# Kernel optimization log

Measured on AMD Instinct MI355X. Metric: run time of the kernel, lower is better.

Reference implementation:

```python
import jax, jax.numpy as jnp
import numpy as np

B, T, K, V, D, H = 16, 512, 32, 512, 64, 128


def setup_inputs() -> dict:
    key = jax.random.key(0)
    ks = jax.random.split(key, 10)
    s = lambda k, shape: jax.random.normal(k, shape, jnp.float32) * 0.05
    sequences = jax.random.randint(ks[0], (B, T), 0, V)
    lengths = jax.random.randint(ks[1], (B,), 1, T + 1)
    return dict(
        sequences=sequences,
        lengths=lengths,
        emb=s(ks[2], (V, D)),
        W1=s(ks[3], (D, H)), b1=jnp.zeros((H,), jnp.float32),
        W2=s(ks[4], (H, K * K)), b2=jnp.zeros((K * K,), jnp.float32),
        E1=s(ks[5], (D, H)), e1=jnp.zeros((H,), jnp.float32),
        E2=s(ks[6], (H, K * V)), e2=jnp.zeros((K * V,), jnp.float32),
        init_logits=s(ks[7], (K,)),
    )


def reference(sequences, lengths, emb, W1, b1, W2, b2, E1, e1, E2, e2, init_logits):
    Bc, Tc = sequences.shape
    # shift inputs: start token 0 followed by sequences[:, :-1]
    inputs = jnp.concatenate(
        [jnp.zeros((Bc, 1), sequences.dtype), sequences[:, :-1]], axis=1)
    x = emb[inputs]                                  # (B,T,D)
    # transition net -> (B,T,K,K) row-normalized in log space
    h1 = jax.nn.relu(x @ W1 + b1)
    log_trans = jax.nn.log_softmax((h1 @ W2 + b2).reshape(Bc, Tc, K, K), axis=-1)
    # emission net -> (B,T,K,V), gather observed-token scores
    h2 = jax.nn.relu(x @ E1 + e1)
    log_emit = jax.nn.log_softmax((h2 @ E2 + e2).reshape(Bc, Tc, K, V), axis=-1)
    tgt = jnp.broadcast_to(sequences[:, :, None, None], (Bc, Tc, K, 1))
    emit_scores = jnp.take_along_axis(log_emit, tgt, axis=3)[..., 0]  # (B,T,K)
    init_lp = jax.nn.log_softmax(init_logits)
    alpha0 = init_lp[None, :] + emit_scores[:, 0]    # (B,K)

    def step(alpha, xs):
        lt, es, t = xs                               # (B,K,K),(B,K),()
        new = jax.nn.logsumexp(alpha[:, :, None] + lt, axis=1) + es
        alpha = jnp.where((t < lengths)[:, None], new, alpha)
        return alpha, None

    xs = (jnp.swapaxes(log_trans, 0, 1)[1:],
          jnp.swapaxes(emit_scores, 0, 1)[1:],
          jnp.arange(1, Tc))
    alpha, _ = jax.lax.scan(step, alpha0, xs)
    return -jax.nn.logsumexp(alpha, axis=1)         # (B,) negative log-likelihood
```

## Files before the change

kernel.cpp:

```cpp
#include <hip/hip_runtime.h>
#include <hip/hip_bf16.h>

#define BB 16
#define TT 512
#define KK 32
#define VV 512
#define DD 64
#define HH 128
#define KV (KK*VV)
#define KKK (KK*KK)

#define INV_LN2 1.4426950408889634f
#define LN2 0.6931471805599453f

typedef unsigned short u16;
typedef __attribute__((ext_vector_type(8))) short short8;
typedef __attribute__((ext_vector_type(8))) unsigned short ushort8;
typedef __attribute__((ext_vector_type(16))) float f32x16;
typedef __attribute__((ext_vector_type(4))) unsigned int uint4v;

__device__ __forceinline__ float fexp2(float x) { return __builtin_amdgcn_exp2f(x); }
__device__ __forceinline__ float flog2(float x) { return __builtin_amdgcn_logf(x); }

__device__ __forceinline__ u16 f2bf(float f) {
  unsigned u = __builtin_bit_cast(unsigned, f);
  u += 0x7FFFu + ((u >> 16) & 1u);
  return (u16)(u >> 16);
}
__device__ __forceinline__ float bf2f(u16 v) {
  return __builtin_bit_cast(float, ((unsigned)v) << 16);
}

__device__ __forceinline__ float es_dot(const u16* __restrict__ erow,
                                        const u16* __restrict__ hrow) {
  float a0 = 0.f, a1 = 0.f, a2 = 0.f, a3 = 0.f;
#pragma unroll
  for (int r = 0; r < 8; ++r) {
    short8 ev = ((const short8*)erow)[r];
    short8 hv = ((const short8*)hrow)[r];
    a0 += bf2f((u16)ev[0]) * bf2f((u16)hv[0]);
    a1 += bf2f((u16)ev[1]) * bf2f((u16)hv[1]);
    a2 += bf2f((u16)ev[2]) * bf2f((u16)hv[2]);
    a3 += bf2f((u16)ev[3]) * bf2f((u16)hv[3]);
    a0 += bf2f((u16)ev[4]) * bf2f((u16)hv[4]);
    a1 += bf2f((u16)ev[5]) * bf2f((u16)hv[5]);
    a2 += bf2f((u16)ev[6]) * bf2f((u16)hv[6]);
    a3 += bf2f((u16)ev[7]) * bf2f((u16)hv[7]);
  }
  return (a0 + a1) + (a2 + a3);
}

__device__ __forceinline__ void mul_step(short8 fr0, short8 fr1, int h,
                                         float* D) {
  float e0[8], e1[8];
#pragma unroll
  for (int i2 = 0; i2 < 4; ++i2) {
    float x0 = __shfl_xor(D[i2], 32);
    float y0 = __shfl_xor(D[4 + i2], 32);
    e0[i2] = (h == 0) ? D[i2] : y0;
    e0[4 + i2] = (h == 0) ? x0 : D[4 + i2];
    float x1 = __shfl_xor(D[8 + i2], 32);
    float y1 = __shfl_xor(D[12 + i2], 32);
    e1[i2] = (h == 0) ? D[8 + i2] : y1;
    e1[4 + i2] = (h == 0) ? x1 : D[12 + i2];
  }
  short8 B0, B1;
#pragma unroll
  for (int e = 0; e < 8; ++e) {
    B0[e] = (short)f2bf(e0[e]);
    B1[e] = (short)f2bf(e1[e]);
  }
  f32x16 dn = {};
  dn = __builtin_amdgcn_mfma_f32_32x32x16_bf16(fr0, B0, dn, 0, 0, 0);
  dn = __builtin_amdgcn_mfma_f32_32x32x16_bf16(fr1, B1, dn, 0, 0, 0);
#pragma unroll
  for (int r = 0; r < 16; ++r) D[r] = dn[r];
}

__device__ __forceinline__ void ident_D(int j, int h, float* D) {
#pragma unroll
  for (int r = 0; r < 16; ++r) D[r] = 0.f;
  if (((j >> 2) & 1) == h) D[(j & 3) | ((j >> 3) << 2)] = 1.0f;
}

__global__ __launch_bounds__(256) void k_prep1(
    const float* __restrict__ E2, u16* __restrict__ E2bT,
    const float* __restrict__ W2, u16* __restrict__ W2T,
    const float* __restrict__ emb, const float* __restrict__ W1,
    const float* __restrict__ b1, const float* __restrict__ E1,
    const float* __restrict__ e1, u16* __restrict__ h1b,
    u16* __restrict__ h2b) {
  __shared__ float tl[32][65];
  __shared__ float embs[16][64];
  int tid = threadIdx.x;
  int bid = blockIdx.x;

  if (bid < 1088) {
    const float* src;
    u16* dst;
    size_t srcld;
    int c0, h0;
    if (bid < 1024) {
      c0 = (bid & 255) * 64;
      h0 = (bid >> 8) * 32;
      src = E2;
      dst = E2bT;
      srcld = KV;
    } else {
      int b2i = bid - 1024;
      c0 = (b2i & 15) * 64;
      h0 = (b2i >> 4) * 32;
      src = W2;
      dst = W2T;
      srcld = KKK;
    }
    int r = tid >> 6, c = tid & 63;
#pragma unroll
    for (int rr = 0; rr < 8; ++rr)
      tl[r * 8 + rr][c] = src[(size_t)(h0 + r * 8 + rr) * srcld + c0 + c];
    __syncthreads();
    int cw = tid >> 3, hb = tid & 7;
#pragma unroll
    for (int pass = 0; pass < 2; ++pass) {
      int cc = pass * 32 + cw;
      unsigned lo = (unsigned)f2bf(tl[hb * 4 + 0][cc]) |
                    ((unsigned)f2bf(tl[hb * 4 + 1][cc]) << 16);
      unsigned hi = (unsigned)f2bf(tl[hb * 4 + 2][cc]) |
                    ((unsigned)f2bf(tl[hb * 4 + 3][cc]) << 16);
      uint2 v;
      v.x = lo;
      v.y = hi;
      *(uint2*)(dst + (size_t)(c0 + cc) * HH + h0 + hb * 4) = v;
    }
    return;
  }

  int u0 = (bid - 1088) * 16;
#pragma unroll
  for (int it = 0; it < 4; ++it) {
    int idx = it * 256 + tid;
    embs[idx >> 6][idx & 63] = emb[u0 * DD + idx];
  }
  __syncthreads();
  int h = tid & 127, tl2 = tid >> 7;
  float b1v = b1[h], e1v = e1[h];
#pragma unroll
  for (int it = 0; it < 8; ++it) {
    int tok = it * 2 + tl2;
    float a1 = b1v, a2 = e1v;
#pragma unroll 8
    for (int d = 0; d < DD; ++d) {
      float xv = embs[tok][d];
      a1 += xv * W1[d * HH + h];
      a2 += xv * E1[d * HH + h];
    }
    h1b[(u0 + tok) * HH + h] = f2bf(fmaxf(a1, 0.f));
    h2b[(u0 + tok) * HH + h] = f2bf(fmaxf(a2, 0.f));
  }
}

__global__ __launch_bounds__(256) void k_transmfma(
    const u16* __restrict__ h1b, const u16* __restrict__ W2T,
    const float* __restrict__ b2, float* __restrict__ ltrans) {
  int i = blockIdx.x;
  int w = threadIdx.x >> 6, l = threadIdx.x & 63;
  int tt = blockIdx.y * 4 + w;
  int u0 = tt * 32;
  int h = l >> 5, j = l & 31;

  f32x16 acc = {};
#pragma unroll
  for (int kh = 0; kh < 8; ++kh) {
    short8 A = *(const short8*)(h1b + (u0 + j) * HH + kh * 16 + h * 8);
    short8 Bf = *(const short8*)(W2T + (i * 32 + j) * HH + kh * 16 + h * 8);
    acc = __builtin_amdgcn_mfma_f32_32x32x16_bf16(A, Bf, acc, 0, 0, 0);
  }
  float b2v = b2[i * 32 + j] * INV_LN2;
  float lgv[16], se[16];
#pragma unroll
  for (int r = 0; r < 16; ++r) {
    lgv[r] = acc[r] * INV_LN2 + b2v;
    se[r] = fexp2(lgv[r]);
  }
#pragma unroll
  for (int r = 0; r < 16; ++r) {
#pragma unroll
    for (int d = 1; d < 32; d <<= 1) se[r] += __shfl_xor(se[r], d);
  }
#pragma unroll
  for (int r = 0; r < 16; ++r) {
    int row = (r & 3) + 8 * (r >> 2) + 4 * h;
    ltrans[(u0 + row) * KKK + j * KK + i] = lgv[r] - flog2(se[r]);
  }
}

__global__ __launch_bounds__(256) void k_emit_lse(
    const u16* __restrict__ h2b, const u16* __restrict__ E2bT,
    const float* __restrict__ e2, float* __restrict__ lse2_tab) {
  int k = blockIdx.x;
  int u0 = blockIdx.y * 32;
  int tid = threadIdx.x;
  int w = tid >> 6, l = tid & 63;
  int h = l >> 5, j = l & 31;
  __shared__ float ls[4 * 32];

  short8 A[8];
#pragma unroll
  for (int kh = 0; kh < 8; ++kh)
    A[kh] = *(const short8*)(h2b + (u0 + j) * HH + kh * 16 + h * 8);

  float s[16];
#pragma unroll
  for (int r = 0; r < 16; ++r) s[r] = 0.f;

#pragma unroll
  for (int c = 0; c < 4; ++c) {
    int ct = w * 4 + c;
    int col = k * 512 + ct * 32 + j;
    const u16* bp = E2bT + (size_t)col * HH + h * 8;
    f32x16 acc = {};
#pragma unroll
    for (int kh = 0; kh < 8; ++kh) {
      short8 Bf = *(const short8*)(bp + kh * 16);
      acc = __builtin_amdgcn_mfma_f32_32x32x16_bf16(A[kh], Bf, acc, 0, 0, 0);
    }
    float e2v = e2[col] * INV_LN2;
#pragma unroll
    for (int r = 0; r < 16; ++r) s[r] += fexp2(acc[r] * INV_LN2 + e2v);
  }
#pragma unroll
  for (int r = 0; r < 16; ++r) {
#pragma unroll
    for (int d = 1; d < 32; d <<= 1) s[r] += __shfl_xor(s[r], d);
  }
  if (j == 0) {
#pragma unroll
    for (int r = 0; r < 16; ++r) {
      int row = (r & 3) + 8 * (r >> 2) + 4 * h;
      ls[w * 32 + row] = s[r];
    }
  }
  __syncthreads();
  if (tid < 32) {
    float total = ls[tid] + ls[32 + tid] + ls[64 + tid] + ls[96 + tid];
    lse2_tab[(u0 + tid) * KK + k] = flog2(total);
  }
}

__global__ __launch_bounds__(256) void k_matprod(
    const int* __restrict__ seq, const int* __restrict__ lengths,
    const float* __restrict__ ltrans, const u16* __restrict__ h2b,
    const u16* __restrict__ E2bT, const float* __restrict__ e2,
    const float* __restrict__ lse2, u16* __restrict__ C1,
    float* __restrict__ s1) {
  __shared__ float tmp[4][32 * 33];
  int w = threadIdx.x >> 6, l = threadIdx.x & 63;
  int c = blockIdx.x * 4 + w;
  int b = c >> 7, t0 = (c & 127) * 4;
  int j = l & 31, h = l >> 5;
  int len = lengths[b];
  len = (len < 1) ? 1 : ((len > TT) ? TT : len);
  const int* sb = seq + b * TT;
  int tlo = (t0 < 1) ? 1 : t0;
  int thi = (t0 + 4 < len) ? (t0 + 4) : len;

  u16* op = C1 + (size_t)c * 1024 + j * 32 + h * 16;
  if (tlo >= thi) {
    ushort8 w0v, w1v;
#pragma unroll
    for (int e = 0; e < 8; ++e) {
      w0v[e] = ((h * 16 + e) == j) ? (u16)0x3F80 : (u16)0;
      w1v[e] = ((h * 16 + 8 + e) == j) ? (u16)0x3F80 : (u16)0;
    }
    *(ushort8*)op = w0v;
    *(ushort8*)(op + 8) = w1v;
    if (l == 0) s1[c] = 0.f;
    return;
  }

  short8 fr0s[4], fr1s[4];
  float sacc = 0.f;
#pragma unroll
  for (int s = 0; s < 4; ++s) {
    int t = t0 + s;
    if (t >= 1 && t < len) {
      int u = sb[t - 1], y = sb[t];
      float dot = es_dot(E2bT + (size_t)(j * VV + y) * HH + h * 64,
                         h2b + u * HH + h * 64);
      dot += __shfl_xor(dot, 32);
      float esj = (dot + e2[j * VV + y]) * INV_LN2 - lse2[u * KK + j];
      float m = esj;
#pragma unroll
      for (int d = 1; d < 32; d <<= 1) m = fmaxf(m, __shfl_xor(m, d));
      sacc += m;
      const float4* p4 = (const float4*)(ltrans + u * KKK + j * KK + h * 16);
      float4 q0 = p4[0], q1 = p4[1], q2 = p4[2], q3 = p4[3];
      float lgv[16] = {q0.x, q0.y, q0.z, q0.w, q1.x, q1.y, q1.z, q1.w,
                       q2.x, q2.y, q2.z, q2.w, q3.x, q3.y, q3.z, q3.w};
      float off = esj - m;
#pragma unroll
      for (int e = 0; e < 16; ++e) lgv[e] += off;
      unsigned pk[8];
#pragma unroll
      for (int p = 0; p < 8; ++p)
        pk[p] = (unsigned)f2bf(fexp2(lgv[2 * p])) |
                ((unsigned)f2bf(fexp2(lgv[2 * p + 1])) << 16);
      unsigned rcv[4];
#pragma unroll
      for (int p = 0; p < 4; ++p)
        rcv[p] = (unsigned)__shfl_xor((int)(h == 0 ? pk[4 + p] : pk[p]), 32);
      unsigned f0[4], f1[4];
#pragma unroll
      for (int p = 0; p < 4; ++p) {
        f0[p] = h == 0 ? pk[p] : rcv[p];
        f1[p] = h == 0 ? rcv[p] : pk[4 + p];
      }
      fr0s[s] = __builtin_bit_cast(short8, (uint4v){f0[0], f0[1], f0[2], f0[3]});
      fr1s[s] = __builtin_bit_cast(short8, (uint4v){f1[0], f1[1], f1[2], f1[3]});
    } else {
      ushort8 i0, i1;
#pragma unroll
      for (int e = 0; e < 8; ++e) {
        i0[e] = ((h * 8 + e) == j) ? (u16)0x3F80 : (u16)0;
        i1[e] = ((16 + h * 8 + e) == j) ? (u16)0x3F80 : (u16)0;
      }
      fr0s[s] = __builtin_bit_cast(short8, i0);
      fr1s[s] = __builtin_bit_cast(short8, i1);
    }
  }

  float D[16];
  ident_D(j, h, D);
#pragma unroll
  for (int s = 0; s < 4; ++s) mul_step(fr0s[s], fr1s[s], h, D);

  float mx = D[0];
#pragma unroll
  for (int r = 1; r < 16; ++r) mx = fmaxf(mx, D[r]);
#pragma unroll
  for (int d = 1; d < 64; d <<= 1) mx = fmaxf(mx, __shfl_xor(mx, d));
  float inv = 1.0f / mx;
#pragma unroll
  for (int r = 0; r < 16; ++r) {
    int row = (r & 3) + 8 * (r >> 2) + 4 * h;
    tmp[w][row * 33 + j] = D[r] * inv;
  }
  ushort8 w0v, w1v;
#pragma unroll
  for (int e = 0; e < 8; ++e) {
    w0v[e] = f2bf(tmp[w][j * 33 + h * 16 + e]);
    w1v[e] = f2bf(tmp[w][j * 33 + h * 16 + 8 + e]);
  }
  *(ushort8*)op = w0v;
  *(ushort8*)(op + 8) = w1v;
  if (l == 0) s1[c] = flog2(mx) + sacc;
}

__global__ __launch_bounds__(512) void k_final2(
    const u16* __restrict__ C1, const float* __restrict__ s1,
    const int* __restrict__ seq, const u16* __restrict__ h2b,
    const u16* __restrict__ E2bT, const float* __restrict__ e2,
    const float* __restrict__ lse2, const float* __restrict__ init_logits,
    float* __restrict__ out) {
  __shared__ u16 mats[8][1024];
  __shared__ float scs[8];
  int b = blockIdx.x;
  int w = threadIdx.x >> 6, l = threadIdx.x & 63;
  int j = l & 31, h = l >> 5;

  float D[16];
  ident_D(j, h, D);
  const u16* base = C1 + ((size_t)b * 128 + w * 16) * 1024;
#pragma unroll
  for (int s = 0; s < 16; ++s) {
    short8 fr0 = *(const short8*)(base + s * 1024 + j * 32 + h * 8);
    short8 fr1 = *(const short8*)(base + s * 1024 + j * 32 + h * 8 + 16);
    mul_step(fr0, fr1, h, D);
  }
  float mx = D[0];
#pragma unroll
  for (int r = 1; r < 16; ++r) mx = fmaxf(mx, D[r]);
#pragma unroll
  for (int d = 1; d < 64; d <<= 1) mx = fmaxf(mx, __shfl_xor(mx, d));
  float inv = 1.0f / mx;
#pragma unroll
  for (int r = 0; r < 16; ++r) {
    int row = (r & 3) + 8 * (r >> 2) + 4 * h;
    mats[w][row * 32 + j] = f2bf(D[r] * inv);
  }
  float si = (l < 16) ? s1[b * 128 + w * 16 + l] : 0.f;
#pragma unroll
  for (int d = 1; d < 64; d <<= 1) si += __shfl_xor(si, d);
  if (l == 0) scs[w] = flog2(mx) + si;
  __syncthreads();

  if (w == 0) {
    float D2[16];
    ident_D(j, h, D2);
#pragma unroll
    for (int s = 0; s < 8; ++s) {
      short8 fr0 = *(const short8*)(&mats[s][j * 32 + h * 8]);
      short8 fr1 = *(const short8*)(&mats[s][j * 32 + h * 8 + 16]);
      mul_step(fr0, fr1, h, D2);
    }
    int y0 = seq[b * TT];
    float dot = es_dot(E2bT + (size_t)(j * VV + y0) * HH + h * 64,
                       h2b + h * 64);
    dot += __shfl_xor(dot, 32);
    float esj = (dot + e2[j * VV + y0]) * INV_LN2 - lse2[j];
    float il = init_logits[j] * INV_LN2;
    float m0 = il;
#pragma unroll
    for (int d = 1; d < 32; d <<= 1) m0 = fmaxf(m0, __shfl_xor(m0, d));
    float s0 = fexp2(il - m0);
#pragma unroll
    for (int d = 1; d < 32; d <<= 1) s0 += __shfl_xor(s0, d);
    float lse0 = m0 + flog2(s0);
    float z = il - lse0 + esj;
    float am = z;
#pragma unroll
    for (int d = 1; d < 32; d <<= 1) am = fmaxf(am, __shfl_xor(am, d));
    float a0 = fexp2(z - am);
    float colsum = 0.f;
#pragma unroll
    for (int r = 0; r < 16; ++r) colsum += D2[r];
    float p = a0 * colsum;
#pragma unroll
    for (int d = 1; d < 64; d <<= 1) p += __shfl_xor(p, d);
    float sct = (l < 8) ? scs[l] : 0.f;
#pragma unroll
    for (int d = 1; d < 64; d <<= 1) sct += __shfl_xor(sct, d);
    if (l == 0) out[b] = -LN2 * (flog2(p) + am + sct);
  }
}

extern "C" void kernel_launch(void* const* d_in, const int* in_sizes, int n_in,
                              void* d_out, int out_size, void* d_ws,
                              size_t ws_size, hipStream_t stream) {
  const int* seq = (const int*)d_in[0];
  const int* lengths = (const int*)d_in[1];
  const float* emb = (const float*)d_in[2];
  const float* W1 = (const float*)d_in[3];
  const float* b1 = (const float*)d_in[4];
  const float* W2 = (const float*)d_in[5];
  const float* b2 = (const float*)d_in[6];
  const float* E1 = (const float*)d_in[7];
  const float* e1 = (const float*)d_in[8];
  const float* E2 = (const float*)d_in[9];
  const float* e2 = (const float*)d_in[10];
  const float* init_logits = (const float*)d_in[11];
  float* out = (float*)d_out;

  char* wsb = (char*)d_ws;
  float* ltrans = (float*)(wsb + 0);
  u16* h2b = (u16*)(wsb + 2097152);
  u16* h1b = (u16*)(wsb + 2228224);
  u16* E2bT = (u16*)(wsb + 2359296);
  u16* W2T = (u16*)(wsb + 6553600);
  float* lse2 = (float*)(wsb + 6815744);
  u16* C1 = (u16*)(wsb + 6881280);
  float* s1 = (float*)(wsb + 11075584);

  k_prep1<<<1120, 256, 0, stream>>>(E2, E2bT, W2, W2T, emb, W1, b1, E1, e1,
                                    h1b, h2b);
  k_transmfma<<<dim3(32, 4), 256, 0, stream>>>(h1b, W2T, b2, ltrans);
  k_emit_lse<<<dim3(32, 16), 256, 0, stream>>>(h2b, E2bT, e2, lse2);
  k_matprod<<<512, 256, 0, stream>>>(seq, lengths, ltrans, h2b, E2bT, e2,
                                     lse2, C1, s1);
  k_final2<<<16, 512, 0, stream>>>(C1, s1, seq, h2b, E2bT, e2, lse2,
                                   init_logits, out);
}
```

Measured before the change: 90.32 us.

## Merge table kernels and fold final reduction into matprod via last-block atomic

```diff
diff --git a/kernel.cpp b/kernel.cpp
--- a/kernel.cpp
+++ b/kernel.cpp
@@ -89,11 +89,12 @@
     const float* __restrict__ emb, const float* __restrict__ W1,
     const float* __restrict__ b1, const float* __restrict__ E1,
     const float* __restrict__ e1, u16* __restrict__ h1b,
-    u16* __restrict__ h2b) {
+    u16* __restrict__ h2b, int* __restrict__ cnt) {
   __shared__ float tl[32][65];
   __shared__ float embs[16][64];
   int tid = threadIdx.x;
   int bid = blockIdx.x;
+  if (bid == 0 && tid < BB) cnt[tid] = 0;
 
   if (bid < 1088) {
     const float* src;
@@ -159,14 +160,69 @@
   }
 }
 
-__global__ __launch_bounds__(256) void k_transmfma(
+__global__ __launch_bounds__(256) void k_tables(
     const u16* __restrict__ h1b, const u16* __restrict__ W2T,
-    const float* __restrict__ b2, float* __restrict__ ltrans) {
-  int i = blockIdx.x;
-  int w = threadIdx.x >> 6, l = threadIdx.x & 63;
-  int tt = blockIdx.y * 4 + w;
+    const float* __restrict__ b2, float* __restrict__ ltrans,
+    const u16* __restrict__ h2b, const u16* __restrict__ E2bT,
+    const float* __restrict__ e2, float* __restrict__ lse2_tab) {
+  __shared__ float ls[4 * 32];
+  int bid = blockIdx.x;
+  int tid = threadIdx.x;
+  int w = tid >> 6, l = tid & 63;
+  int h = l >> 5, j = l & 31;
+
+  if (bid < 512) {
+    int k = bid & 31;
+    int u0 = (bid >> 5) * 32;
+
+    short8 A[8];
+#pragma unroll
+    for (int kh = 0; kh < 8; ++kh)
+      A[kh] = *(const short8*)(h2b + (u0 + j) * HH + kh * 16 + h * 8);
+
+    float s[16];
+#pragma unroll
+    for (int r = 0; r < 16; ++r) s[r] = 0.f;
+
+#pragma unroll
+    for (int c = 0; c < 4; ++c) {
+      int ct = w * 4 + c;
+      int col = k * 512 + ct * 32 + j;
+      const u16* bp = E2bT + (size_t)col * HH + h * 8;
+      f32x16 acc = {};
+#pragma unroll
+      for (int kh = 0; kh < 8; ++kh) {
+        short8 Bf = *(const short8*)(bp + kh * 16);
+        acc = __builtin_amdgcn_mfma_f32_32x32x16_bf16(A[kh], Bf, acc, 0, 0, 0);
+      }
+      float e2v = e2[col] * INV_LN2;
+#pragma unroll
+      for (int r = 0; r < 16; ++r) s[r] += fexp2(acc[r] * INV_LN2 + e2v);
+    }
+#pragma unroll
+    for (int r = 0; r < 16; ++r) {
+#pragma unroll
+      for (int d = 1; d < 32; d <<= 1) s[r] += __shfl_xor(s[r], d);
+    }
+    if (j == 0) {
+#pragma unroll
+      for (int r = 0; r < 16; ++r) {
+        int row = (r & 3) + 8 * (r >> 2) + 4 * h;
+        ls[w * 32 + row] = s[r];
+      }
+    }
+    __syncthreads();
+    if (tid < 32) {
+      float total = ls[tid] + ls[32 + tid] + ls[64 + tid] + ls[96 + tid];
+      lse2_tab[(u0 + tid) * KK + k] = flog2(total);
+    }
+    return;
+  }
+
+  int t2 = bid - 512;
+  int i = t2 & 31;
+  int tt = (t2 >> 5) * 4 + w;
   int u0 = tt * 32;
-  int h = l >> 5, j = l & 31;
 
   f32x16 acc = {};
 #pragma unroll
@@ -191,59 +247,6 @@
   for (int r = 0; r < 16; ++r) {
     int row = (r & 3) + 8 * (r >> 2) + 4 * h;
     ltrans[(u0 + row) * KKK + j * KK + i] = lgv[r] - flog2(se[r]);
-  }
-}
-
-__global__ __launch_bounds__(256) void k_emit_lse(
-    const u16* __restrict__ h2b, const u16* __restrict__ E2bT,
-    const float* __restrict__ e2, float* __restrict__ lse2_tab) {
-  int k = blockIdx.x;
-  int u0 = blockIdx.y * 32;
-  int tid = threadIdx.x;
-  int w = tid >> 6, l = tid & 63;
-  int h = l >> 5, j = l & 31;
-  __shared__ float ls[4 * 32];
-
-  short8 A[8];
-#pragma unroll
-  for (int kh = 0; kh < 8; ++kh)
-    A[kh] = *(const short8*)(h2b + (u0 + j) * HH + kh * 16 + h * 8);
-
-  float s[16];
-#pragma unroll
-  for (int r = 0; r < 16; ++r) s[r] = 0.f;
-
-#pragma unroll
-  for (int c = 0; c < 4; ++c) {
-    int ct = w * 4 + c;
-    int col = k * 512 + ct * 32 + j;
-    const u16* bp = E2bT + (size_t)col * HH + h * 8;
-    f32x16 acc = {};
-#pragma unroll
-    for (int kh = 0; kh < 8; ++kh) {
-      short8 Bf = *(const short8*)(bp + kh * 16);
-      acc = __builtin_amdgcn_mfma_f32_32x32x16_bf16(A[kh], Bf, acc, 0, 0, 0);
-    }
-    float e2v = e2[col] * INV_LN2;
-#pragma unroll
-    for (int r = 0; r < 16; ++r) s[r] += fexp2(acc[r] * INV_LN2 + e2v);
-  }
-#pragma unroll
-  for (int r = 0; r < 16; ++r) {
-#pragma unroll
-    for (int d = 1; d < 32; d <<= 1) s[r] += __shfl_xor(s[r], d);
-  }
-  if (j == 0) {
-#pragma unroll
-    for (int r = 0; r < 16; ++r) {
-      int row = (r & 3) + 8 * (r >> 2) + 4 * h;
-      ls[w * 32 + row] = s[r];
-    }
-  }
-  __syncthreads();
-  if (tid < 32) {
-    float total = ls[tid] + ls[32 + tid] + ls[64 + tid] + ls[96 + tid];
-    lse2_tab[(u0 + tid) * KK + k] = flog2(total);
   }
 }
 
@@ -252,17 +255,21 @@
     const float* __restrict__ ltrans, const u16* __restrict__ h2b,
     const u16* __restrict__ E2bT, const float* __restrict__ e2,
     const float* __restrict__ lse2, u16* __restrict__ C1,
-    float* __restrict__ s1) {
+    float* __restrict__ s1, int* __restrict__ cnt,
+    const float* __restrict__ init_logits, float* __restrict__ out) {
   __shared__ float tmp[4][32 * 33];
+  __shared__ u16 mats[4][1024];
+  __shared__ float scs[4];
+  __shared__ int lastflag;
   int w = threadIdx.x >> 6, l = threadIdx.x & 63;
   int c = blockIdx.x * 4 + w;
-  int b = c >> 7, t0 = (c & 127) * 4;
+  int b = c >> 6, t0 = (c & 63) * 8;
   int j = l & 31, h = l >> 5;
   int len = lengths[b];
   len = (len < 1) ? 1 : ((len > TT) ? TT : len);
   const int* sb = seq + b * TT;
   int tlo = (t0 < 1) ? 1 : t0;
-  int thi = (t0 + 4 < len) ? (t0 + 4) : len;
+  int thi = (t0 + 8 < len) ? (t0 + 8) : len;
 
   u16* op = C1 + (size_t)c * 1024 + j * 32 + h * 16;
   if (tlo >= thi) {
@@ -275,102 +282,100 @@
     *(ushort8*)op = w0v;
     *(ushort8*)(op + 8) = w1v;
     if (l == 0) s1[c] = 0.f;
-    return;
-  }
-
-  short8 fr0s[4], fr1s[4];
-  float sacc = 0.f;
-#pragma unroll
-  for (int s = 0; s < 4; ++s) {
-    int t = t0 + s;
-    if (t >= 1 && t < len) {
-      int u = sb[t - 1], y = sb[t];
-      float dot = es_dot(E2bT + (size_t)(j * VV + y) * HH + h * 64,
-                         h2b + u * HH + h * 64);
-      dot += __shfl_xor(dot, 32);
-      float esj = (dot + e2[j * VV + y]) * INV_LN2 - lse2[u * KK + j];
-      float m = esj;
-#pragma unroll
-      for (int d = 1; d < 32; d <<= 1) m = fmaxf(m, __shfl_xor(m, d));
-      sacc += m;
-      const float4* p4 = (const float4*)(ltrans + u * KKK + j * KK + h * 16);
-      float4 q0 = p4[0], q1 = p4[1], q2 = p4[2], q3 = p4[3];
-      float lgv[16] = {q0.x, q0.y, q0.z, q0.w, q1.x, q1.y, q1.z, q1.w,
-                       q2.x, q2.y, q2.z, q2.w, q3.x, q3.y, q3.z, q3.w};
-      float off = esj - m;
-#pragma unroll
-      for (int e = 0; e < 16; ++e) lgv[e] += off;
-      unsigned pk[8];
-#pragma unroll
-      for (int p = 0; p < 8; ++p)
-        pk[p] = (unsigned)f2bf(fexp2(lgv[2 * p])) |
-                ((unsigned)f2bf(fexp2(lgv[2 * p + 1])) << 16);
-      unsigned rcv[4];
-#pragma unroll
-      for (int p = 0; p < 4; ++p)
-        rcv[p] = (unsigned)__shfl_xor((int)(h == 0 ? pk[4 + p] : pk[p]), 32);
-      unsigned f0[4], f1[4];
-#pragma unroll
-      for (int p = 0; p < 4; ++p) {
-        f0[p] = h == 0 ? pk[p] : rcv[p];
-        f1[p] = h == 0 ? rcv[p] : pk[4 + p];
+  } else {
+    short8 fr0s[8], fr1s[8];
+    float sacc = 0.f;
+#pragma unroll
+    for (int s = 0; s < 8; ++s) {
+      int t = t0 + s;
+      if (t >= 1 && t < len) {
+        int u = sb[t - 1], y = sb[t];
+        float dot = es_dot(E2bT + (size_t)(j * VV + y) * HH + h * 64,
+                           h2b + u * HH + h * 64);
+        dot += __shfl_xor(dot, 32);
+        float esj = (dot + e2[j * VV + y]) * INV_LN2 - lse2[u * KK + j];
+        float m = esj;
+#pragma unroll
+        for (int d = 1; d < 32; d <<= 1) m = fmaxf(m, __shfl_xor(m, d));
+        sacc += m;
+        const float4* p4 = (const float4*)(ltrans + u * KKK + j * KK + h * 16);
+        float4 q0 = p4[0], q1 = p4[1], q2 = p4[2], q3 = p4[3];
+        float lgv[16] = {q0.x, q0.y, q0.z, q0.w, q1.x, q1.y, q1.z, q1.w,
+                         q2.x, q2.y, q2.z, q2.w, q3.x, q3.y, q3.z, q3.w};
+        float off = esj - m;
+#pragma unroll
+        for (int e = 0; e < 16; ++e) lgv[e] += off;
+        unsigned pk[8];
+#pragma unroll
+        for (int p = 0; p < 8; ++p)
+          pk[p] = (unsigned)f2bf(fexp2(lgv[2 * p])) |
+                  ((unsigned)f2bf(fexp2(lgv[2 * p + 1])) << 16);
+        unsigned rcv[4];
+#pragma unroll
+        for (int p = 0; p < 4; ++p)
+          rcv[p] = (unsigned)__shfl_xor((int)(h == 0 ? pk[4 + p] : pk[p]), 32);
+        unsigned f0[4], f1[4];
+#pragma unroll
+        for (int p = 0; p < 4; ++p) {
+          f0[p] = h == 0 ? pk[p] : rcv[p];
+          f1[p] = h == 0 ? rcv[p] : pk[4 + p];
+        }
+        fr0s[s] =
+            __builtin_bit_cast(short8, (uint4v){f0[0], f0[1], f0[2], f0[3]});
+        fr1s[s] =
+            __builtin_bit_cast(short8, (uint4v){f1[0], f1[1], f1[2], f1[3]});
+      } else {
+        ushort8 i0, i1;
+#pragma unroll
+        for (int e = 0; e < 8; ++e) {
+          i0[e] = ((h * 8 + e) == j) ? (u16)0x3F80 : (u16)0;
+          i1[e] = ((16 + h * 8 + e) == j) ? (u16)0x3F80 : (u16)0;
+        }
+        fr0s[s] = __builtin_bit_cast(short8, i0);
+        fr1s[s] = __builtin_bit_cast(short8, i1);
       }
-      fr0s[s] = __builtin_bit_cast(short8, (uint4v){f0[0], f0[1], f0[2], f0[3]});
-      fr1s[s] = __builtin_bit_cast(short8, (uint4v){f1[0], f1[1], f1[2], f1[3]});
-    } else {
-      ushort8 i0, i1;
-#pragma unroll
-      for (int e = 0; e < 8; ++e) {
-        i0[e] = ((h * 8 + e) == j) ? (u16)0x3F80 : (u16)0;
-        i1[e] = ((16 + h * 8 + e) == j) ? (u16)0x3F80 : (u16)0;
-      }
-      fr0s[s] = __builtin_bit_cast(short8, i0);
-      fr1s[s] = __builtin_bit_cast(short8, i1);
-    }
-  }
+    }
+
+    float D[16];
+    ident_D(j, h, D);
+#pragma unroll
+    for (int s = 0; s < 8; ++s) mul_step(fr0s[s], fr1s[s], h, D);
+
+    float mx = D[0];
+#pragma unroll
+    for (int r = 1; r < 16; ++r) mx = fmaxf(mx, D[r]);
+#pragma unroll
+    for (int d = 1; d < 64; d <<= 1) mx = fmaxf(mx, __shfl_xor(mx, d));
+    float inv = 1.0f / mx;
+#pragma unroll
+    for (int r = 0; r < 16; ++r) {
+      int row = (r & 3) + 8 * (r >> 2) + 4 * h;
+      tmp[w][row * 33 + j] = D[r] * inv;
+    }
+    ushort8 w0v, w1v;
+#pragma unroll
+    for (int e = 0; e < 8; ++e) {
+      w0v[e] = f2bf(tmp[w][j * 33 + h * 16 + e]);
+      w1v[e] = f2bf(tmp[w][j * 33 + h * 16 + 8 + e]);
+    }
+    *(ushort8*)op = w0v;
+    *(ushort8*)(op + 8) = w1v;
+    if (l == 0) s1[c] = flog2(mx) + sacc;
+  }
+
+  __threadfence();
+  __syncthreads();
+  if (threadIdx.x == 0) {
+    int old = atomicAdd(&cnt[b], 1);
+    lastflag = (old == 15) ? 1 : 0;
+  }
+  __syncthreads();
+  if (!lastflag) return;
+  __threadfence();
 
   float D[16];
   ident_D(j, h, D);
-#pragma unroll
-  for (int s = 0; s < 4; ++s) mul_step(fr0s[s], fr1s[s], h, D);
-
-  float mx = D[0];
-#pragma unroll
-  for (int r = 1; r < 16; ++r) mx = fmaxf(mx, D[r]);
-#pragma unroll
-  for (int d = 1; d < 64; d <<= 1) mx = fmaxf(mx, __shfl_xor(mx, d));
-  float inv = 1.0f / mx;
-#pragma unroll
-  for (int r = 0; r < 16; ++r) {
-    int row = (r & 3) + 8 * (r >> 2) + 4 * h;
-    tmp[w][row * 33 + j] = D[r] * inv;
-  }
-  ushort8 w0v, w1v;
-#pragma unroll
-  for (int e = 0; e < 8; ++e) {
-    w0v[e] = f2bf(tmp[w][j * 33 + h * 16 + e]);
-    w1v[e] = f2bf(tmp[w][j * 33 + h * 16 + 8 + e]);
-  }
-  *(ushort8*)op = w0v;
-  *(ushort8*)(op + 8) = w1v;
-  if (l == 0) s1[c] = flog2(mx) + sacc;
-}
-
-__global__ __launch_bounds__(512) void k_final2(
-    const u16* __restrict__ C1, const float* __restrict__ s1,
-    const int* __restrict__ seq, const u16* __restrict__ h2b,
-    const u16* __restrict__ E2bT, const float* __restrict__ e2,
-    const float* __restrict__ lse2, const float* __restrict__ init_logits,
-    float* __restrict__ out) {
-  __shared__ u16 mats[8][1024];
-  __shared__ float scs[8];
-  int b = blockIdx.x;
-  int w = threadIdx.x >> 6, l = threadIdx.x & 63;
-  int j = l & 31, h = l >> 5;
-
-  float D[16];
-  ident_D(j, h, D);
-  const u16* base = C1 + ((size_t)b * 128 + w * 16) * 1024;
+  const u16* base = C1 + ((size_t)b * 64 + w * 16) * 1024;
 #pragma unroll
   for (int s = 0; s < 16; ++s) {
     short8 fr0 = *(const short8*)(base + s * 1024 + j * 32 + h * 8);
@@ -388,7 +393,7 @@
     int row = (r & 3) + 8 * (r >> 2) + 4 * h;
     mats[w][row * 32 + j] = f2bf(D[r] * inv);
   }
-  float si = (l < 16) ? s1[b * 128 + w * 16 + l] : 0.f;
+  float si = (l < 16) ? s1[b * 64 + w * 16 + l] : 0.f;
 #pragma unroll
   for (int d = 1; d < 64; d <<= 1) si += __shfl_xor(si, d);
   if (l == 0) scs[w] = flog2(mx) + si;
@@ -398,7 +403,7 @@
     float D2[16];
     ident_D(j, h, D2);
 #pragma unroll
-    for (int s = 0; s < 8; ++s) {
+    for (int s = 0; s < 4; ++s) {
       short8 fr0 = *(const short8*)(&mats[s][j * 32 + h * 8]);
       short8 fr1 = *(const short8*)(&mats[s][j * 32 + h * 8 + 16]);
       mul_step(fr0, fr1, h, D2);
@@ -427,7 +432,7 @@
     float p = a0 * colsum;
 #pragma unroll
     for (int d = 1; d < 64; d <<= 1) p += __shfl_xor(p, d);
-    float sct = (l < 8) ? scs[l] : 0.f;
+    float sct = (l < 4) ? scs[l] : 0.f;
 #pragma unroll
     for (int d = 1; d < 64; d <<= 1) sct += __shfl_xor(sct, d);
     if (l == 0) out[b] = -LN2 * (flog2(p) + am + sct);
@@ -459,14 +464,12 @@
   u16* W2T = (u16*)(wsb + 6553600);
   float* lse2 = (float*)(wsb + 6815744);
   u16* C1 = (u16*)(wsb + 6881280);
-  float* s1 = (float*)(wsb + 11075584);
+  float* s1 = (float*)(wsb + 8978432);
+  int* cnt = (int*)(wsb + 8982528);
 
   k_prep1<<<1120, 256, 0, stream>>>(E2, E2bT, W2, W2T, emb, W1, b1, E1, e1,
-                                    h1b, h2b);
-  k_transmfma<<<dim3(32, 4), 256, 0, stream>>>(h1b, W2T, b2, ltrans);
-  k_emit_lse<<<dim3(32, 16), 256, 0, stream>>>(h2b, E2bT, e2, lse2);
-  k_matprod<<<512, 256, 0, stream>>>(seq, lengths, ltrans, h2b, E2bT, e2,
-                                     lse2, C1, s1);
-  k_final2<<<16, 512, 0, stream>>>(C1, s1, seq, h2b, E2bT, e2, lse2,
-                                   init_logits, out);
-}
+                                    h1b, h2b, cnt);
+  k_tables<<<640, 256, 0, stream>>>(h1b, W2T, b2, ltrans, h2b, E2bT, e2, lse2);
+  k_matprod<<<256, 256, 0, stream>>>(seq, lengths, ltrans, h2b, E2bT, e2,
+                                     lse2, C1, s1, cnt, init_logits, out);
+}
```

Result: slower. 111.3 us (+23.2%).

## Merge transition and emission-LSE kernels, add y-major E2 copy, lengthen matprod chunks

Applied to the files above, without the earlier changes.

```diff
diff --git a/kernel.cpp b/kernel.cpp
--- a/kernel.cpp
+++ b/kernel.cpp
@@ -85,11 +85,11 @@
 
 __global__ __launch_bounds__(256) void k_prep1(
     const float* __restrict__ E2, u16* __restrict__ E2bT,
-    const float* __restrict__ W2, u16* __restrict__ W2T,
-    const float* __restrict__ emb, const float* __restrict__ W1,
-    const float* __restrict__ b1, const float* __restrict__ E1,
-    const float* __restrict__ e1, u16* __restrict__ h1b,
-    u16* __restrict__ h2b) {
+    u16* __restrict__ E2yT, const float* __restrict__ W2,
+    u16* __restrict__ W2T, const float* __restrict__ emb,
+    const float* __restrict__ W1, const float* __restrict__ b1,
+    const float* __restrict__ E1, const float* __restrict__ e1,
+    u16* __restrict__ h1b, u16* __restrict__ h2b) {
   __shared__ float tl[32][65];
   __shared__ float embs[16][64];
   int tid = threadIdx.x;
@@ -100,7 +100,8 @@
     u16* dst;
     size_t srcld;
     int c0, h0;
-    if (bid < 1024) {
+    int isE2 = (bid < 1024);
+    if (isE2) {
       c0 = (bid & 255) * 64;
       h0 = (bid >> 8) * 32;
       src = E2;
@@ -130,7 +131,12 @@
       uint2 v;
       v.x = lo;
       v.y = hi;
-      *(uint2*)(dst + (size_t)(c0 + cc) * HH + h0 + hb * 4) = v;
+      int col = c0 + cc;
+      *(uint2*)(dst + (size_t)col * HH + h0 + hb * 4) = v;
+      if (isE2) {
+        int k = col >> 9, y = col & 511;
+        *(uint2*)(E2yT + ((size_t)y * KK + k) * HH + h0 + hb * 4) = v;
+      }
     }
     return;
   }
@@ -159,14 +165,69 @@
   }
 }
 
-__global__ __launch_bounds__(256) void k_transmfma(
+__global__ __launch_bounds__(256) void k_tables(
     const u16* __restrict__ h1b, const u16* __restrict__ W2T,
-    const float* __restrict__ b2, float* __restrict__ ltrans) {
-  int i = blockIdx.x;
-  int w = threadIdx.x >> 6, l = threadIdx.x & 63;
-  int tt = blockIdx.y * 4 + w;
+    const float* __restrict__ b2, float* __restrict__ ltrans,
+    const u16* __restrict__ h2b, const u16* __restrict__ E2bT,
+    const float* __restrict__ e2, float* __restrict__ lse2_tab) {
+  __shared__ float ls[4 * 32];
+  int bid = blockIdx.x;
+  int tid = threadIdx.x;
+  int w = tid >> 6, l = tid & 63;
+  int h = l >> 5, j = l & 31;
+
+  if (bid < 512) {
+    int k = bid & 31;
+    int u0 = (bid >> 5) * 32;
+
+    short8 A[8];
+#pragma unroll
+    for (int kh = 0; kh < 8; ++kh)
+      A[kh] = *(const short8*)(h2b + (u0 + j) * HH + kh * 16 + h * 8);
+
+    float s[16];
+#pragma unroll
+    for (int r = 0; r < 16; ++r) s[r] = 0.f;
+
+#pragma unroll
+    for (int c = 0; c < 4; ++c) {
+      int ct = w * 4 + c;
+      int col = k * 512 + ct * 32 + j;
+      const u16* bp = E2bT + (size_t)col * HH + h * 8;
+      f32x16 acc = {};
+#pragma unroll
+      for (int kh = 0; kh < 8; ++kh) {
+        short8 Bf = *(const short8*)(bp + kh * 16);
+        acc = __builtin_amdgcn_mfma_f32_32x32x16_bf16(A[kh], Bf, acc, 0, 0, 0);
+      }
+      float e2v = e2[col] * INV_LN2;
+#pragma unroll
+      for (int r = 0; r < 16; ++r) s[r] += fexp2(acc[r] * INV_LN2 + e2v);
+    }
+#pragma unroll
+    for (int r = 0; r < 16; ++r) {
+#pragma unroll
+      for (int d = 1; d < 32; d <<= 1) s[r] += __shfl_xor(s[r], d);
+    }
+    if (j == 0) {
+#pragma unroll
+      for (int r = 0; r < 16; ++r) {
+        int row = (r & 3) + 8 * (r >> 2) + 4 * h;
+        ls[w * 32 + row] = s[r];
+      }
+    }
+    __syncthreads();
+    if (tid < 32) {
+      float total = ls[tid] + ls[32 + tid] + ls[64 + tid] + ls[96 + tid];
+      lse2_tab[(u0 + tid) * KK + k] = flog2(total);
+    }
+    return;
+  }
+
+  int t2 = bid - 512;
+  int i = t2 & 31;
+  int tt = (t2 >> 5) * 4 + w;
   int u0 = tt * 32;
-  int h = l >> 5, j = l & 31;
 
   f32x16 acc = {};
 #pragma unroll
@@ -194,75 +255,22 @@
   }
 }
 
-__global__ __launch_bounds__(256) void k_emit_lse(
-    const u16* __restrict__ h2b, const u16* __restrict__ E2bT,
-    const float* __restrict__ e2, float* __restrict__ lse2_tab) {
-  int k = blockIdx.x;
-  int u0 = blockIdx.y * 32;
-  int tid = threadIdx.x;
-  int w = tid >> 6, l = tid & 63;
-  int h = l >> 5, j = l & 31;
-  __shared__ float ls[4 * 32];
-
-  short8 A[8];
-#pragma unroll
-  for (int kh = 0; kh < 8; ++kh)
-    A[kh] = *(const short8*)(h2b + (u0 + j) * HH + kh * 16 + h * 8);
-
-  float s[16];
-#pragma unroll
-  for (int r = 0; r < 16; ++r) s[r] = 0.f;
-
-#pragma unroll
-  for (int c = 0; c < 4; ++c) {
-    int ct = w * 4 + c;
-    int col = k * 512 + ct * 32 + j;
-    const u16* bp = E2bT + (size_t)col * HH + h * 8;
-    f32x16 acc = {};
-#pragma unroll
-    for (int kh = 0; kh < 8; ++kh) {
-      short8 Bf = *(const short8*)(bp + kh * 16);
-      acc = __builtin_amdgcn_mfma_f32_32x32x16_bf16(A[kh], Bf, acc, 0, 0, 0);
-    }
-    float e2v = e2[col] * INV_LN2;
-#pragma unroll
-    for (int r = 0; r < 16; ++r) s[r] += fexp2(acc[r] * INV_LN2 + e2v);
-  }
-#pragma unroll
-  for (int r = 0; r < 16; ++r) {
-#pragma unroll
-    for (int d = 1; d < 32; d <<= 1) s[r] += __shfl_xor(s[r], d);
-  }
-  if (j == 0) {
-#pragma unroll
-    for (int r = 0; r < 16; ++r) {
-      int row = (r & 3) + 8 * (r >> 2) + 4 * h;
-      ls[w * 32 + row] = s[r];
-    }
-  }
-  __syncthreads();
-  if (tid < 32) {
-    float total = ls[tid] + ls[32 + tid] + ls[64 + tid] + ls[96 + tid];
-    lse2_tab[(u0 + tid) * KK + k] = flog2(total);
-  }
-}
-
 __global__ __launch_bounds__(256) void k_matprod(
     const int* __restrict__ seq, const int* __restrict__ lengths,
     const float* __restrict__ ltrans, const u16* __restrict__ h2b,
-    const u16* __restrict__ E2bT, const float* __restrict__ e2,
+    const u16* __restrict__ E2yT, const float* __restrict__ e2,
     const float* __restrict__ lse2, u16* __restrict__ C1,
     float* __restrict__ s1) {
   __shared__ float tmp[4][32 * 33];
   int w = threadIdx.x >> 6, l = threadIdx.x & 63;
   int c = blockIdx.x * 4 + w;
-  int b = c >> 7, t0 = (c & 127) * 4;
+  int b = c >> 6, t0 = (c & 63) * 8;
   int j = l & 31, h = l >> 5;
   int len = lengths[b];
   len = (len < 1) ? 1 : ((len > TT) ? TT : len);
   const int* sb = seq + b * TT;
   int tlo = (t0 < 1) ? 1 : t0;
-  int thi = (t0 + 4 < len) ? (t0 + 4) : len;
+  int thi = (t0 + 8 < len) ? (t0 + 8) : len;
 
   u16* op = C1 + (size_t)c * 1024 + j * 32 + h * 16;
   if (tlo >= thi) {
@@ -278,14 +286,14 @@
     return;
   }
 
-  short8 fr0s[4], fr1s[4];
+  short8 fr0s[8], fr1s[8];
   float sacc = 0.f;
 #pragma unroll
-  for (int s = 0; s < 4; ++s) {
+  for (int s = 0; s < 8; ++s) {
     int t = t0 + s;
     if (t >= 1 && t < len) {
       int u = sb[t - 1], y = sb[t];
-      float dot = es_dot(E2bT + (size_t)(j * VV + y) * HH + h * 64,
+      float dot = es_dot(E2yT + ((size_t)y * KK + j) * HH + h * 64,
                          h2b + u * HH + h * 64);
       dot += __shfl_xor(dot, 32);
       float esj = (dot + e2[j * VV + y]) * INV_LN2 - lse2[u * KK + j];
@@ -332,7 +340,7 @@
   float D[16];
   ident_D(j, h, D);
 #pragma unroll
-  for (int s = 0; s < 4; ++s) mul_step(fr0s[s], fr1s[s], h, D);
+  for (int s = 0; s < 8; ++s) mul_step(fr0s[s], fr1s[s], h, D);
 
   float mx = D[0];
 #pragma unroll
@@ -359,7 +367,7 @@
 __global__ __launch_bounds__(512) void k_final2(
     const u16* __restrict__ C1, const float* __restrict__ s1,
     const int* __restrict__ seq, const u16* __restrict__ h2b,
-    const u16* __restrict__ E2bT, const float* __restrict__ e2,
+    const u16* __restrict__ E2yT, const float* __restrict__ e2,
     const float* __restrict__ lse2, const float* __restrict__ init_logits,
     float* __restrict__ out) {
   __shared__ u16 mats[8][1024];
@@ -370,9 +378,9 @@
 
   float D[16];
   ident_D(j, h, D);
-  const u16* base = C1 + ((size_t)b * 128 + w * 16) * 1024;
-#pragma unroll
-  for (int s = 0; s < 16; ++s) {
+  const u16* base = C1 + ((size_t)b * 64 + w * 8) * 1024;
+#pragma unroll
+  for (int s = 0; s < 8; ++s) {
     short8 fr0 = *(const short8*)(base + s * 1024 + j * 32 + h * 8);
     short8 fr1 = *(const short8*)(base + s * 1024 + j * 32 + h * 8 + 16);
     mul_step(fr0, fr1, h, D);
@@ -388,7 +396,7 @@
     int row = (r & 3) + 8 * (r >> 2) + 4 * h;
     mats[w][row * 32 + j] = f2bf(D[r] * inv);
   }
-  float si = (l < 16) ? s1[b * 128 + w * 16 + l] : 0.f;
+  float si = (l < 8) ? s1[b * 64 + w * 8 + l] : 0.f;
 #pragma unroll
   for (int d = 1; d < 64; d <<= 1) si += __shfl_xor(si, d);
   if (l == 0) scs[w] = flog2(mx) + si;
@@ -404,7 +412,7 @@
       mul_step(fr0, fr1, h, D2);
     }
     int y0 = seq[b * TT];
-    float dot = es_dot(E2bT + (size_t)(j * VV + y0) * HH + h * 64,
+    float dot = es_dot(E2yT + ((size_t)y0 * KK + j) * HH + h * 64,
                        h2b + h * 64);
     dot += __shfl_xor(dot, 32);
     float esj = (dot + e2[j * VV + y0]) * INV_LN2 - lse2[j];
@@ -459,14 +467,14 @@
   u16* W2T = (u16*)(wsb + 6553600);
   float* lse2 = (float*)(wsb + 6815744);
   u16* C1 = (u16*)(wsb + 6881280);
-  float* s1 = (float*)(wsb + 11075584);
-
-  k_prep1<<<1120, 256, 0, stream>>>(E2, E2bT, W2, W2T, emb, W1, b1, E1, e1,
-                                    h1b, h2b);
-  k_transmfma<<<dim3(32, 4), 256, 0, stream>>>(h1b, W2T, b2, ltrans);
-  k_emit_lse<<<dim3(32, 16), 256, 0, stream>>>(h2b, E2bT, e2, lse2);
-  k_matprod<<<512, 256, 0, stream>>>(seq, lengths, ltrans, h2b, E2bT, e2,
+  float* s1 = (float*)(wsb + 8978432);
+  u16* E2yT = (u16*)(wsb + 8982528);
+
+  k_prep1<<<1120, 256, 0, stream>>>(E2, E2bT, E2yT, W2, W2T, emb, W1, b1, E1,
+                                    e1, h1b, h2b);
+  k_tables<<<640, 256, 0, stream>>>(h1b, W2T, b2, ltrans, h2b, E2bT, e2, lse2);
+  k_matprod<<<256, 256, 0, stream>>>(seq, lengths, ltrans, h2b, E2yT, e2,
                                      lse2, C1, s1);
-  k_final2<<<16, 512, 0, stream>>>(C1, s1, seq, h2b, E2bT, e2, lse2,
+  k_final2<<<16, 512, 0, stream>>>(C1, s1, seq, h2b, E2yT, e2, lse2,
                                    init_logits, out);
 }
```

After: 83.11 us. 8.0% less time.
